# Kernel optimization log

Measured on AMD Instinct MI355X. Metric: run time of the kernel, lower is better.

Reference implementation:

```python
import jax, jax.numpy as jnp
import numpy as np

B, C, H, W = 8, 256, 64, 64   # C = in_channels(64) * no_g(4)
DQK = 8                        # max(in_channels//8, no_g) = max(8,4)


def setup_inputs() -> dict:
    key = jax.random.key(0)
    ks = jax.random.split(key, 8)
    s_in = 1.0 / np.sqrt(C)
    return {
        "x": jax.random.normal(ks[0], (B, C, H, W), dtype=jnp.float32),
        "wq": jax.random.normal(ks[1], (DQK, C), dtype=jnp.float32) * s_in,
        "bq": jax.random.normal(ks[2], (DQK,), dtype=jnp.float32) * 0.01,
        "wk": jax.random.normal(ks[3], (DQK, C), dtype=jnp.float32) * s_in,
        "bk": jax.random.normal(ks[4], (DQK,), dtype=jnp.float32) * 0.01,
        "wv": jax.random.normal(ks[5], (C, C), dtype=jnp.float32) * s_in,
        "bv": jax.random.normal(ks[6], (C,), dtype=jnp.float32) * 0.01,
        "gamma": jax.random.normal(ks[7], (1,), dtype=jnp.float32) * 0.5,
    }


def reference(x, wq, bq, wk, bk, wv, bv, gamma):
    b, c, h, w = x.shape
    n = h * w
    xf = x.reshape(b, c, n)                                   # B,C,N
    q = (jnp.einsum('bcn,qc->bqn', xf, wq) + bq[None, :, None])  # B,DQK,N (1x1 conv)
    k = (jnp.einsum('bcn,qc->bqn', xf, wk) + bk[None, :, None])  # B,DQK,N
    v = (jnp.einsum('bcn,oc->bon', xf, wv) + bv[None, :, None])  # B,C,N
    energy = jnp.einsum('bdn,bdm->bnm', q, k)                 # B,N,N (no scale, as in source)
    attn = jax.nn.softmax(energy, axis=-1)                    # softmax over last dim
    # out[b,c,m] = sum_n v[b,c,n] * attn[b,m,n]  (bmm(V, A^T))
    out = jnp.einsum('bcn,bmn->bcm', v, attn).reshape(b, c, h, w)
    return gamma[0] * out + x
```

## Files before the change

### kernel.cpp

```cpp
#include <hip/hip_runtime.h>
#include <math.h>

namespace {

constexpr int B_ = 8;
constexpr int C_ = 256;
constexpr int N_ = 4096;

constexpr int TM = 64;
constexpr int TN = 128;
constexpr int NCH = N_ / TN;
constexpr int PSTRIDE = 136;
constexpr float LOG2E = 1.4426950408889634f;

constexpr int VBLK = C_ * 16;

typedef __attribute__((ext_vector_type(8))) short short8;
typedef __attribute__((ext_vector_type(16))) float float16;

__device__ inline unsigned short f2bf(float f) {
  unsigned u = __float_as_uint(f);
  u += 0x7FFFu + ((u >> 16) & 1u);
  return (unsigned short)(u >> 16);
}
__device__ inline float bf2f(unsigned short h) {
  return __uint_as_float(((unsigned)h) << 16);
}

__global__ __launch_bounds__(256) void prep_kernel(
    const float* __restrict__ wv, const float* __restrict__ wq,
    const float* __restrict__ wk,
    unsigned short* __restrict__ wv_bf, unsigned short* __restrict__ wqk_bf) {
  const int i = blockIdx.x * 256 + threadIdx.x;
  wv_bf[i] = f2bf(wv[i]);
  if (i < 2048) {
    const int d = i >> 8, c = i & 255;
    const float qL = wq[i] * LOG2E;
    const unsigned short hq = f2bf(qL);
    wqk_bf[d * 256 + c]        = hq;
    wqk_bf[(d + 8) * 256 + c]  = f2bf(qL - bf2f(hq));
    const float kv = wk[i];
    const unsigned short hk = f2bf(kv);
    wqk_bf[(d + 16) * 256 + c] = hk;
    wqk_bf[(d + 24) * 256 + c] = f2bf(kv - bf2f(hk));
  }
}

__device__ inline short8 xfrag(const float* xs, int c0, int n) {
  short8 r;
  #pragma unroll
  for (int i = 0; i < 8; ++i) r[i] = (short)f2bf(xs[(c0 + i) * 32 + n]);
  return r;
}

__global__ __launch_bounds__(256, 4) void proj_kernel(
    const float* __restrict__ x,
    const float* __restrict__ bq, const float* __restrict__ bk,
    const unsigned short* __restrict__ wqk_bf,
    const unsigned short* __restrict__ wv_bf, const float* __restrict__ bv,
    unsigned short* __restrict__ q_t, unsigned short* __restrict__ k_th,
    unsigned short* __restrict__ k_tl, unsigned short* __restrict__ v)
{
  __shared__ float xs[256 * 32];

  const int b = blockIdx.y;
  const int n0 = blockIdx.x * 32;
  const int tid = threadIdx.x;
  const int w = tid >> 6, l = tid & 63;
  const int l31 = l & 31, lh = l >> 5;

  {
    const int c_off = l >> 5, nn = l & 31;
    const float* gp = x + ((size_t)b * C_ + w * 64 + c_off) * N_ + n0 + nn;
    const float* lp = xs + (w * 64) * 32;
    #pragma unroll
    for (int i = 0; i < 64; i += 2) {
      __builtin_amdgcn_global_load_lds(
          (const __attribute__((address_space(1))) void*)(gp + (size_t)i * N_),
          (__attribute__((address_space(3))) void*)(lp + i * 32), 4, 0, 0);
    }
  }
  __syncthreads();

  if (w == 0) {
    float16 sacc;
    #pragma unroll
    for (int r = 0; r < 16; ++r) sacc[r] = 0.f;
    for (int ks = 0; ks < 16; ++ks) {
      const short8 a = *reinterpret_cast<const short8*>(
          wqk_bf + l31 * 256 + ks * 16 + lh * 8);
      const short8 bfg = xfrag(xs, ks * 16 + lh * 8, l31);
      sacc = __builtin_amdgcn_mfma_f32_32x32x16_bf16(a, bfg, sacc, 0, 0, 0);
    }
    const size_t gn = (size_t)b * N_ + n0 + l31;
    #pragma unroll
    for (int r = 0; r < 4; ++r) {
      const int d = r + 4 * lh;
      const float qv = sacc[r] + sacc[r + 4] + bq[d] * LOG2E;
      const unsigned short hq = f2bf(qv);
      q_t[gn * 16 + d]     = hq;
      q_t[gn * 16 + 8 + d] = f2bf(qv - bf2f(hq));
      const float kv = sacc[r + 8] + sacc[r + 12] + bk[d];
      const unsigned short hk = f2bf(kv);
      k_th[gn * 8 + d] = hk;
      k_tl[gn * 8 + d] = f2bf(kv - bf2f(hk));
    }
  }

  float16 acc[2];
  #pragma unroll
  for (int mi = 0; mi < 2; ++mi)
    #pragma unroll
    for (int r = 0; r < 16; ++r) acc[mi][r] = 0.f;

  for (int ks = 0; ks < 16; ++ks) {
    short8 af[2];
    #pragma unroll
    for (int mi = 0; mi < 2; ++mi)
      af[mi] = *reinterpret_cast<const short8*>(
          wv_bf + (w * 64 + mi * 32 + l31) * C_ + ks * 16 + lh * 8);
    const short8 bfg = xfrag(xs, ks * 16 + lh * 8, l31);
    #pragma unroll
    for (int mi = 0; mi < 2; ++mi)
      acc[mi] = __builtin_amdgcn_mfma_f32_32x32x16_bf16(af[mi], bfg, acc[mi], 0, 0, 0);
  }

  #pragma unroll
  for (int mi = 0; mi < 2; ++mi)
    #pragma unroll
    for (int r = 0; r < 16; ++r) {
      const int c = w * 64 + mi * 32 + (r & 3) + 8 * (r >> 2) + 4 * lh;
      const int n = n0 + l31;
      const int nblk = n >> 4, nin = n & 15;
      v[(((size_t)b * (N_ / 16) + nblk) * C_ + c) * 16 + nin] =
          f2bf(acc[mi][r] + bv[c]);
    }
}

__global__ __launch_bounds__(512, 4) void attn_kernel(
    const unsigned short* __restrict__ q_t, const unsigned short* __restrict__ k_th,
    const unsigned short* __restrict__ k_tl, const unsigned short* __restrict__ v,
    const float* __restrict__ x, const float* __restrict__ gamma,
    float* __restrict__ out)
{
  __shared__ __align__(16) unsigned short ps[2][TM][PSTRIDE];
  __shared__ float rsp[4][TM];
  __shared__ float rsn[TM];

  const int b = blockIdx.x;
  const int m0 = blockIdx.y * TM;
  const int tid = threadIdx.x;
  const int w = tid >> 6;
  const int l = tid & 63;
  const int l31 = l & 31, lh = l >> 5;
  const int mt = w >> 2, nt = w & 3;
  const int ncol = nt * 32 + l31;

  const short8 aq = *reinterpret_cast<const short8*>(
      q_t + ((size_t)b * N_ + m0 + 32 * mt + l31) * 16 + lh * 8);

  const unsigned short* vlane =
      v + ((size_t)b * (N_ / 16)) * VBLK + (size_t)(w * 32 + l31) * 16 + lh * 8;
  const unsigned short* kbh = k_th + (size_t)b * N_ * 8;
  const unsigned short* kbl = k_tl + (size_t)b * N_ * 8;

  float16 o0, o1;
  float rsum[16];
  #pragma unroll
  for (int r = 0; r < 16; ++r) { o0[r] = 0.f; o1[r] = 0.f; rsum[r] = 0.f; }

  short8 af[8];
  #pragma unroll
  for (int g = 0; g < 8; ++g)
    af[g] = *reinterpret_cast<const short8*>(vlane + (size_t)g * VBLK);
  {
    const short8 bh = *reinterpret_cast<const short8*>(kbh + (size_t)ncol * 8);
    const short8 bl = *reinterpret_cast<const short8*>(kbl + (size_t)ncol * 8);
    float16 s;
    #pragma unroll
    for (int r = 0; r < 16; ++r) s[r] = 0.f;
    s = __builtin_amdgcn_mfma_f32_32x32x16_bf16(aq, bh, s, 0, 0, 0);
    s = __builtin_amdgcn_mfma_f32_32x32x16_bf16(aq, bl, s, 0, 0, 0);
    #pragma unroll
    for (int r = 0; r < 16; ++r) {
      const float e = exp2f(s[r]);
      rsum[r] += e;
      const int mrow = 32 * mt + (r & 3) + 8 * (r >> 2) + 4 * lh;
      ps[0][mrow][ncol] = f2bf(e);
    }
  }
  __syncthreads();

  for (int nc = 0; nc < NCH; ++nc) {
    const int buf = nc & 1;
    const bool more = (nc + 1) < NCH;
    const int nc1 = more ? (nc + 1) : 0;
    const int n1 = nc1 * TN;

    const short8 bh = *reinterpret_cast<const short8*>(kbh + (size_t)(n1 + ncol) * 8);
    const short8 bl = *reinterpret_cast<const short8*>(kbl + (size_t)(n1 + ncol) * 8);

    #pragma unroll
    for (int ks = 0; ks < 8; ++ks) {
      const short8 p0 = *reinterpret_cast<const short8*>(&ps[buf][l31][ks * 16 + lh * 8]);
      const short8 p1 = *reinterpret_cast<const short8*>(&ps[buf][32 + l31][ks * 16 + lh * 8]);
      o0 = __builtin_amdgcn_mfma_f32_32x32x16_bf16(af[ks], p0, o0, 0, 0, 0);
      o1 = __builtin_amdgcn_mfma_f32_32x32x16_bf16(af[ks], p1, o1, 0, 0, 0);
      af[ks] = *reinterpret_cast<const short8*>(vlane + (size_t)(nc1 * 8 + ks) * VBLK);
    }

    if (more) {
      float16 s;
      #pragma unroll
      for (int r = 0; r < 16; ++r) s[r] = 0.f;
      s = __builtin_amdgcn_mfma_f32_32x32x16_bf16(aq, bh, s, 0, 0, 0);
      s = __builtin_amdgcn_mfma_f32_32x32x16_bf16(aq, bl, s, 0, 0, 0);
      #pragma unroll
      for (int r = 0; r < 16; ++r) {
        const float e = exp2f(s[r]);
        rsum[r] += e;
        const int mrow = 32 * mt + (r & 3) + 8 * (r >> 2) + 4 * lh;
        ps[buf ^ 1][mrow][ncol] = f2bf(e);
      }
    }
    __syncthreads();
  }

  #pragma unroll
  for (int r = 0; r < 16; ++r) {
    float ss = rsum[r];
    #pragma unroll
    for (int off = 16; off >= 1; off >>= 1) ss += __shfl_xor(ss, off);
    rsum[r] = ss;
  }
  if (l31 == 0) {
    #pragma unroll
    for (int r = 0; r < 16; ++r) {
      const int mrow = 32 * mt + (r & 3) + 8 * (r >> 2) + 4 * lh;
      rsp[nt][mrow] = rsum[r];
    }
  }
  __syncthreads();
  if (tid < TM) rsn[tid] = rsp[0][tid] + rsp[1][tid] + rsp[2][tid] + rsp[3][tid];
  __syncthreads();

  const float g = gamma[0];
  const float t0 = g / rsn[l31];
  const float t1 = g / rsn[32 + l31];
  #pragma unroll
  for (int r = 0; r < 16; ++r) {
    const int c = 32 * w + (r & 3) + 8 * (r >> 2) + 4 * lh;
    const size_t i0 = ((size_t)b * C_ + c) * N_ + m0 + l31;
    out[i0]      = fmaf(o0[r], t0, x[i0]);
    out[i0 + 32] = fmaf(o1[r], t1, x[i0 + 32]);
  }
}

}

extern "C" void kernel_launch(void* const* d_in, const int* in_sizes, int n_in,
                              void* d_out, int out_size, void* d_ws, size_t ws_size,
                              hipStream_t stream) {
  const float* x     = (const float*)d_in[0];
  const float* wq    = (const float*)d_in[1];
  const float* bq    = (const float*)d_in[2];
  const float* wk    = (const float*)d_in[3];
  const float* bk    = (const float*)d_in[4];
  const float* wv    = (const float*)d_in[5];
  const float* bv    = (const float*)d_in[6];
  const float* gamma = (const float*)d_in[7];
  float* out = (float*)d_out;

  char* p = (char*)d_ws;
  unsigned short* q_t    = (unsigned short*)p;  p += (size_t)B_ * N_ * 16 * 2;
  unsigned short* k_th   = (unsigned short*)p;  p += (size_t)B_ * N_ * 8 * 2;
  unsigned short* k_tl   = (unsigned short*)p;  p += (size_t)B_ * N_ * 8 * 2;
  unsigned short* wv_bf  = (unsigned short*)p;  p += (size_t)C_ * C_ * 2;
  unsigned short* wqk_bf = (unsigned short*)p;  p += (size_t)32 * C_ * 2;
  unsigned short* v      = (unsigned short*)p;

  prep_kernel<<<dim3(C_ * C_ / 256), 256, 0, stream>>>(wv, wq, wk, wv_bf, wqk_bf);
  proj_kernel<<<dim3(N_ / 32, B_), 256, 0, stream>>>(x, bq, bk, wqk_bf, wv_bf, bv,
                                                     q_t, k_th, k_tl, v);
  attn_kernel<<<dim3(B_, N_ / TM), 512, 0, stream>>>(q_t, k_th, k_tl, v, x, gamma, out);
}
```

Before: 213.4 us.

## Transpose energy MFMA so softmax rows live per lane, pack bf16 stores

The energy MFMA operands are swapped (K as A, Q as B), so each lane holds a single query row across many key columns. The row sum then becomes one scalar per lane, reduced with a single cross-half shuffle instead of 16 five-step shuffle reductions. P tiles are converted with packed hardware bf16 conversion and written as 8-byte vector stores instead of scalar 2-byte stores. Separately, the x staging in the projection kernel uses 16-byte global-to-LDS loads instead of 4-byte ones, which cuts the instruction count for that load.

```diff
diff --git a/kernel.cpp b/kernel.cpp
--- a/kernel.cpp
+++ b/kernel.cpp
@@ -70,14 +70,13 @@
   const int l31 = l & 31, lh = l >> 5;
 
   {
-    const int c_off = l >> 5, nn = l & 31;
-    const float* gp = x + ((size_t)b * C_ + w * 64 + c_off) * N_ + n0 + nn;
-    const float* lp = xs + (w * 64) * 32;
-    #pragma unroll
-    for (int i = 0; i < 64; i += 2) {
+    const int r8 = l >> 3, c4 = (l & 7) * 4;
+    const float* gp = x + ((size_t)b * C_ + w * 64 + r8) * N_ + n0 + c4;
+    #pragma unroll
+    for (int i = 0; i < 64; i += 8) {
       __builtin_amdgcn_global_load_lds(
           (const __attribute__((address_space(1))) void*)(gp + (size_t)i * N_),
-          (__attribute__((address_space(3))) void*)(lp + i * 32), 4, 0, 0);
+          (__attribute__((address_space(3))) void*)(xs + (w * 64 + i) * 32), 16, 0, 0);
     }
   }
   __syncthreads();
@@ -154,39 +153,46 @@
   const int l = tid & 63;
   const int l31 = l & 31, lh = l >> 5;
   const int mt = w >> 2, nt = w & 3;
-  const int ncol = nt * 32 + l31;
-
-  const short8 aq = *reinterpret_cast<const short8*>(
-      q_t + ((size_t)b * N_ + m0 + 32 * mt + l31) * 16 + lh * 8);
+  const int nrow = nt * 32 + l31;
+  const int mcol = 32 * mt + l31;
+
+  const size_t qoff = ((size_t)b * N_ + m0 + mcol) * 16;
+  const short8 qh = *reinterpret_cast<const short8*>(q_t + qoff);
+  const short8 ql = *reinterpret_cast<const short8*>(q_t + qoff + 8);
+
+  const unsigned short* kb = (lh ? k_tl : k_th) + (size_t)b * N_ * 8;
 
   const unsigned short* vlane =
       v + ((size_t)b * (N_ / 16)) * VBLK + (size_t)(w * 32 + l31) * 16 + lh * 8;
-  const unsigned short* kbh = k_th + (size_t)b * N_ * 8;
-  const unsigned short* kbl = k_tl + (size_t)b * N_ * 8;
 
   float16 o0, o1;
-  float rsum[16];
-  #pragma unroll
-  for (int r = 0; r < 16; ++r) { o0[r] = 0.f; o1[r] = 0.f; rsum[r] = 0.f; }
+  #pragma unroll
+  for (int r = 0; r < 16; ++r) { o0[r] = 0.f; o1[r] = 0.f; }
+  float rsum = 0.f;
 
   short8 af[8];
   #pragma unroll
   for (int g = 0; g < 8; ++g)
     af[g] = *reinterpret_cast<const short8*>(vlane + (size_t)g * VBLK);
   {
-    const short8 bh = *reinterpret_cast<const short8*>(kbh + (size_t)ncol * 8);
-    const short8 bl = *reinterpret_cast<const short8*>(kbl + (size_t)ncol * 8);
+    const short8 kf = *reinterpret_cast<const short8*>(kb + (size_t)nrow * 8);
     float16 s;
     #pragma unroll
     for (int r = 0; r < 16; ++r) s[r] = 0.f;
-    s = __builtin_amdgcn_mfma_f32_32x32x16_bf16(aq, bh, s, 0, 0, 0);
-    s = __builtin_amdgcn_mfma_f32_32x32x16_bf16(aq, bl, s, 0, 0, 0);
-    #pragma unroll
-    for (int r = 0; r < 16; ++r) {
-      const float e = exp2f(s[r]);
-      rsum[r] += e;
-      const int mrow = 32 * mt + (r & 3) + 8 * (r >> 2) + 4 * lh;
-      ps[0][mrow][ncol] = f2bf(e);
+    s = __builtin_amdgcn_mfma_f32_32x32x16_bf16(kf, qh, s, 0, 0, 0);
+    s = __builtin_amdgcn_mfma_f32_32x32x16_bf16(kf, ql, s, 0, 0, 0);
+    unsigned short* prow = &ps[0][mcol][nt * 32 + lh * 4];
+    #pragma unroll
+    for (int g = 0; g < 4; ++g) {
+      const float e0 = exp2f(s[4 * g + 0]);
+      const float e1 = exp2f(s[4 * g + 1]);
+      const float e2 = exp2f(s[4 * g + 2]);
+      const float e3 = exp2f(s[4 * g + 3]);
+      rsum += (e0 + e1) + (e2 + e3);
+      uint2 pk;
+      asm("v_cvt_pk_bf16_f32 %0, %1, %2" : "=v"(pk.x) : "v"(e0), "v"(e1));
+      asm("v_cvt_pk_bf16_f32 %0, %1, %2" : "=v"(pk.y) : "v"(e2), "v"(e3));
+      *reinterpret_cast<uint2*>(prow + g * 8) = pk;
     }
   }
   __syncthreads();
@@ -197,8 +203,7 @@
     const int nc1 = more ? (nc + 1) : 0;
     const int n1 = nc1 * TN;
 
-    const short8 bh = *reinterpret_cast<const short8*>(kbh + (size_t)(n1 + ncol) * 8);
-    const short8 bl = *reinterpret_cast<const short8*>(kbl + (size_t)(n1 + ncol) * 8);
+    const short8 kf = *reinterpret_cast<const short8*>(kb + (size_t)(n1 + nrow) * 8);
 
     #pragma unroll
     for (int ks = 0; ks < 8; ++ks) {
@@ -213,33 +218,27 @@
       float16 s;
       #pragma unroll
       for (int r = 0; r < 16; ++r) s[r] = 0.f;
-      s = __builtin_amdgcn_mfma_f32_32x32x16_bf16(aq, bh, s, 0, 0, 0);
-      s = __builtin_amdgcn_mfma_f32_32x32x16_bf16(aq, bl, s, 0, 0, 0);
+      s = __builtin_amdgcn_mfma_f32_32x32x16_bf16(kf, qh, s, 0, 0, 0);
+      s = __builtin_amdgcn_mfma_f32_32x32x16_bf16(kf, ql, s, 0, 0, 0);
+      unsigned short* prow = &ps[buf ^ 1][mcol][nt * 32 + lh * 4];
       #pragma unroll
-      for (int r = 0; r < 16; ++r) {
-        const float e = exp2f(s[r]);
-        rsum[r] += e;
-        const int mrow = 32 * mt + (r & 3) + 8 * (r >> 2) + 4 * lh;
-        ps[buf ^ 1][mrow][ncol] = f2bf(e);
+      for (int g = 0; g < 4; ++g) {
+        const float e0 = exp2f(s[4 * g + 0]);
+        const float e1 = exp2f(s[4 * g + 1]);
+        const float e2 = exp2f(s[4 * g + 2]);
+        const float e3 = exp2f(s[4 * g + 3]);
+        rsum += (e0 + e1) + (e2 + e3);
+        uint2 pk;
+        asm("v_cvt_pk_bf16_f32 %0, %1, %2" : "=v"(pk.x) : "v"(e0), "v"(e1));
+        asm("v_cvt_pk_bf16_f32 %0, %1, %2" : "=v"(pk.y) : "v"(e2), "v"(e3));
+        *reinterpret_cast<uint2*>(prow + g * 8) = pk;
       }
     }
     __syncthreads();
   }
 
-  #pragma unroll
-  for (int r = 0; r < 16; ++r) {
-    float ss = rsum[r];
-    #pragma unroll
-    for (int off = 16; off >= 1; off >>= 1) ss += __shfl_xor(ss, off);
-    rsum[r] = ss;
-  }
-  if (l31 == 0) {
-    #pragma unroll
-    for (int r = 0; r < 16; ++r) {
-      const int mrow = 32 * mt + (r & 3) + 8 * (r >> 2) + 4 * lh;
-      rsp[nt][mrow] = rsum[r];
-    }
-  }
+  rsum += __shfl_xor(rsum, 32);
+  if (l < 32) rsp[nt][mcol] = rsum;
   __syncthreads();
   if (tid < TM) rsn[tid] = rsp[0][tid] + rsp[1][tid] + rsp[2][tid] + rsp[3][tid];
   __syncthreads();
```

New measurement: 206.1 us. -3.4%, faster.
